# Optimization experiments

Hardware: AMD Instinct MI355X
Metric: run time of the kernel (lower is better)

The kernel has to match this reference:

```python
import jax, jax.numpy as jnp
import numpy as np

EMBED = 1024
HEAD = 64
CTX = 2048


def setup_inputs() -> dict:
    key = jax.random.key(0)
    ks = jax.random.split(key, 7)
    scale = 1.0 / np.sqrt(EMBED)
    return {
        "x": jax.random.normal(ks[0], (8, CTX, EMBED), dtype=jnp.float32),
        "Wq": jax.random.normal(ks[1], (EMBED, HEAD), dtype=jnp.float32) * scale,
        "bq": jax.random.normal(ks[2], (HEAD,), dtype=jnp.float32) * 0.01,
        "Wk": jax.random.normal(ks[3], (EMBED, HEAD), dtype=jnp.float32) * scale,
        "bk": jax.random.normal(ks[4], (HEAD,), dtype=jnp.float32) * 0.01,
        "Wv": jax.random.normal(ks[5], (EMBED, HEAD), dtype=jnp.float32) * scale,
        "bv": jax.random.normal(ks[6], (HEAD,), dtype=jnp.float32) * 0.01,
    }


def reference(x, Wq, bq, Wk, bk, Wv, bv):
    # x: [B, T, E]
    q = x @ Wq + bq  # [B, T, H]
    k = x @ Wk + bk
    v = x @ Wv + bv
    scores = jnp.einsum("bqh,bkh->bqk", q, k) / jnp.sqrt(jnp.float32(HEAD))
    T = x.shape[1]
    causal = jnp.tril(jnp.ones((T, T), dtype=bool))
    scores = jnp.where(causal, scores, -jnp.inf)
    attn = jax.nn.softmax(scores, axis=-1)  # dropout=0.0 -> identity
    out = jnp.einsum("bqk,bkh->bqh", attn, v)
    return out
```

## Files before the change

kernel.cpp:

```cpp
#include <hip/hip_runtime.h>
#include <math.h>
#include <stdint.h>

#define BDIM 8
#define TDIM 2048
#define EDIM 1024
#define HDIM 64
#define NCHUNK 144

typedef short bf16x8 __attribute__((ext_vector_type(8)));
typedef float f32x4 __attribute__((ext_vector_type(4)));

__device__ __forceinline__ unsigned short f2bf(float f) {
    uint32_t u = __builtin_bit_cast(uint32_t, f);
    u += 0x7fffu + ((u >> 16) & 1u);
    return (unsigned short)(u >> 16);
}

__global__ __launch_bounds__(256) void prep_w(
    const float* __restrict__ Wq, const float* __restrict__ Wk,
    const float* __restrict__ Wv,
    unsigned short* __restrict__ WqT, unsigned short* __restrict__ WkT,
    unsigned short* __restrict__ WvT)
{
    int id = blockIdx.x * 256 + threadIdx.x;
    int e = id >> 6, h = id & 63;
    int oi = h * EDIM + e;
    WqT[oi] = f2bf(Wq[id]);
    WkT[oi] = f2bf(Wk[id]);
    WvT[oi] = f2bf(Wv[id]);
}

__global__ __launch_bounds__(256) void proj_kernel(
    const float* __restrict__ x,
    const unsigned short* __restrict__ WqT, const unsigned short* __restrict__ WkT,
    const unsigned short* __restrict__ WvT,
    const float* __restrict__ bq, const float* __restrict__ bk,
    const float* __restrict__ bv,
    unsigned short* __restrict__ Qb, unsigned short* __restrict__ Kb,
    unsigned short* __restrict__ VbT)
{
    __shared__ unsigned short Xs[64][72];
    __shared__ unsigned short Wqs[64][72];
    __shared__ unsigned short Wks[64][72];
    __shared__ unsigned short Wvs[64][72];

    const int t = threadIdx.x;
    const int lane = t & 63, w = t >> 6, quad = lane >> 4, ln = lane & 15;
    const int row0 = blockIdx.x * 64;
    const int sr = t >> 2;
    const int sc = (t & 3) << 4;

    f32x4 accq[4], acck[4], accv[4];
#pragma unroll
    for (int j = 0; j < 4; ++j) {
        accq[j] = (f32x4)(0.f); acck[j] = (f32x4)(0.f); accv[j] = (f32x4)(0.f);
    }

    for (int kt = 0; kt < EDIM / 64; ++kt) {
        __syncthreads();
        const float* xp = &x[(size_t)(row0 + sr) * EDIM + kt * 64 + sc];
        float4 x0 = *(const float4*)(xp);
        float4 x1 = *(const float4*)(xp + 4);
        float4 x2 = *(const float4*)(xp + 8);
        float4 x3 = *(const float4*)(xp + 12);
        bf16x8 xb0, xb1;
        xb0[0]=(short)f2bf(x0.x); xb0[1]=(short)f2bf(x0.y); xb0[2]=(short)f2bf(x0.z); xb0[3]=(short)f2bf(x0.w);
        xb0[4]=(short)f2bf(x1.x); xb0[5]=(short)f2bf(x1.y); xb0[6]=(short)f2bf(x1.z); xb0[7]=(short)f2bf(x1.w);
        xb1[0]=(short)f2bf(x2.x); xb1[1]=(short)f2bf(x2.y); xb1[2]=(short)f2bf(x2.z); xb1[3]=(short)f2bf(x2.w);
        xb1[4]=(short)f2bf(x3.x); xb1[5]=(short)f2bf(x3.y); xb1[6]=(short)f2bf(x3.z); xb1[7]=(short)f2bf(x3.w);
        *(bf16x8*)&Xs[sr][sc]     = xb0;
        *(bf16x8*)&Xs[sr][sc + 8] = xb1;
        size_t wo = (size_t)sr * EDIM + kt * 64 + sc;
        *(bf16x8*)&Wqs[sr][sc]     = *(const bf16x8*)&WqT[wo];
        *(bf16x8*)&Wqs[sr][sc + 8] = *(const bf16x8*)&WqT[wo + 8];
        *(bf16x8*)&Wks[sr][sc]     = *(const bf16x8*)&WkT[wo];
        *(bf16x8*)&Wks[sr][sc + 8] = *(const bf16x8*)&WkT[wo + 8];
        *(bf16x8*)&Wvs[sr][sc]     = *(const bf16x8*)&WvT[wo];
        *(bf16x8*)&Wvs[sr][sc + 8] = *(const bf16x8*)&WvT[wo + 8];
        __syncthreads();

        bf16x8 xa0 = *(const bf16x8*)&Xs[16 * w + ln][8 * quad];
        bf16x8 xa1 = *(const bf16x8*)&Xs[16 * w + ln][32 + 8 * quad];
#pragma unroll
        for (int j = 0; j < 4; ++j) {
            bf16x8 w0, w1;
            w0 = *(const bf16x8*)&Wqs[16 * j + ln][8 * quad];
            w1 = *(const bf16x8*)&Wqs[16 * j + ln][32 + 8 * quad];
            accq[j] = __builtin_amdgcn_mfma_f32_16x16x32_bf16(xa0, w0, accq[j], 0, 0, 0);
            accq[j] = __builtin_amdgcn_mfma_f32_16x16x32_bf16(xa1, w1, accq[j], 0, 0, 0);
            w0 = *(const bf16x8*)&Wks[16 * j + ln][8 * quad];
            w1 = *(const bf16x8*)&Wks[16 * j + ln][32 + 8 * quad];
            acck[j] = __builtin_amdgcn_mfma_f32_16x16x32_bf16(xa0, w0, acck[j], 0, 0, 0);
            acck[j] = __builtin_amdgcn_mfma_f32_16x16x32_bf16(xa1, w1, acck[j], 0, 0, 0);
            w0 = *(const bf16x8*)&Wvs[16 * j + ln][8 * quad];
            w1 = *(const bf16x8*)&Wvs[16 * j + ln][32 + 8 * quad];
            accv[j] = __builtin_amdgcn_mfma_f32_16x16x32_bf16(xa0, w0, accv[j], 0, 0, 0);
            accv[j] = __builtin_amdgcn_mfma_f32_16x16x32_bf16(xa1, w1, accv[j], 0, 0, 0);
        }
    }

#pragma unroll
    for (int j = 0; j < 4; ++j) {
        int col = 16 * j + ln;
        float bqv = bq[col], bkv = bk[col], bvv = bv[col];
#pragma unroll
        for (int r = 0; r < 4; ++r) {
            size_t row = (size_t)(row0 + 16 * w + 4 * quad + r);
            Qb[row * HDIM + col] = f2bf(accq[j][r] + bqv);
            Kb[row * HDIM + col] = f2bf(acck[j][r] + bkv);
            int bb = (int)(row >> 11);
            int tr = (int)(row & 2047);
            VbT[((size_t)bb * HDIM + col) * TDIM + tr] = f2bf(accv[j][r] + bvv);
        }
    }
}

__global__ __launch_bounds__(256) void attn_partial(
    const unsigned short* __restrict__ Qb, const unsigned short* __restrict__ Kb,
    const unsigned short* __restrict__ VbT,
    float* __restrict__ PO, float* __restrict__ Pm, float* __restrict__ Pl)
{
    __shared__ unsigned short Ks[64][72];
    __shared__ unsigned short VsT[64][72];
    __shared__ unsigned short Ps[64][72];

    const int t = threadIdx.x;
    const int lane = t & 63, w = t >> 6, quad = lane >> 4, ln = lane & 15;
    const int f = blockIdx.x;
    const int b = blockIdx.y;

    int g = 0;
    while (f >= 2 * (g + 1) * (g + 2)) ++g;
    const int r_  = f - 2 * g * (g + 1);
    const int iq  = 4 * g + r_ / (g + 1);
    const int ch  = r_ % (g + 1);

    const int q0 = iq * 64;
    const size_t base = (size_t)b * TDIM * HDIM;
    const int sr = t >> 2;
    const int sc = (t & 3) << 4;

    const size_t qrow = base + (size_t)(q0 + 16 * w + ln) * HDIM;
    bf16x8 qa0 = *(const bf16x8*)&Qb[qrow + 8 * quad];
    bf16x8 qa1 = *(const bf16x8*)&Qb[qrow + 32 + 8 * quad];

    f32x4 od[4];
#pragma unroll
    for (int j = 0; j < 4; ++j) od[j] = (f32x4)(0.f);
    float mrow[4], lrow[4];
#pragma unroll
    for (int r = 0; r < 4; ++r) { mrow[r] = -INFINITY; lrow[r] = 0.f; }

    const float scale = 0.125f;
    int j1 = 4 * ch + 3; if (j1 > iq) j1 = iq;

    for (int jt = 4 * ch; jt <= j1; ++jt) {
        __syncthreads();
        {
            size_t ko = base + (size_t)(jt * 64 + sr) * HDIM + sc;
            *(bf16x8*)&Ks[sr][sc]     = *(const bf16x8*)&Kb[ko];
            *(bf16x8*)&Ks[sr][sc + 8] = *(const bf16x8*)&Kb[ko + 8];
            const unsigned short* vrow =
                &VbT[((size_t)b * HDIM + sr) * TDIM + jt * 64 + sc];
            *(bf16x8*)&VsT[sr][sc]     = *(const bf16x8*)vrow;
            *(bf16x8*)&VsT[sr][sc + 8] = *(const bf16x8*)(vrow + 8);
        }
        __syncthreads();

        f32x4 s[4];
#pragma unroll
        for (int j = 0; j < 4; ++j) {
            bf16x8 kb0 = *(const bf16x8*)&Ks[16 * j + ln][8 * quad];
            bf16x8 kb1 = *(const bf16x8*)&Ks[16 * j + ln][32 + 8 * quad];
            s[j] = (f32x4)(0.f);
            s[j] = __builtin_amdgcn_mfma_f32_16x16x32_bf16(qa0, kb0, s[j], 0, 0, 0);
            s[j] = __builtin_amdgcn_mfma_f32_16x16x32_bf16(qa1, kb1, s[j], 0, 0, 0);
        }

        if (jt == iq) {
#pragma unroll
            for (int j = 0; j < 4; ++j) {
                int kg = jt * 64 + 16 * j + ln;
#pragma unroll
                for (int r = 0; r < 4; ++r) {
                    int qg = q0 + 16 * w + 4 * quad + r;
                    s[j][r] = (kg <= qg) ? s[j][r] * scale : -INFINITY;
                }
            }
        } else {
#pragma unroll
            for (int j = 0; j < 4; ++j)
#pragma unroll
                for (int r = 0; r < 4; ++r) s[j][r] *= scale;
        }

        float mx[4];
#pragma unroll
        for (int r = 0; r < 4; ++r)
            mx[r] = fmaxf(fmaxf(s[0][r], s[1][r]), fmaxf(s[2][r], s[3][r]));
#pragma unroll
        for (int d = 1; d < 16; d <<= 1)
#pragma unroll
            for (int r = 0; r < 4; ++r)
                mx[r] = fmaxf(mx[r], __shfl_xor(mx[r], d));

        float al[4], rs[4];
#pragma unroll
        for (int r = 0; r < 4; ++r) {
            float mn = fmaxf(mrow[r], mx[r]);
            al[r] = __expf(mrow[r] - mn);
            mrow[r] = mn;
            float p0 = __expf(s[0][r] - mn);
            float p1 = __expf(s[1][r] - mn);
            float p2 = __expf(s[2][r] - mn);
            float p3 = __expf(s[3][r] - mn);
            s[0][r] = p0; s[1][r] = p1; s[2][r] = p2; s[3][r] = p3;
            rs[r] = (p0 + p1) + (p2 + p3);
        }
#pragma unroll
        for (int d = 1; d < 16; d <<= 1)
#pragma unroll
            for (int r = 0; r < 4; ++r)
                rs[r] += __shfl_xor(rs[r], d);
#pragma unroll
        for (int r = 0; r < 4; ++r) lrow[r] = lrow[r] * al[r] + rs[r];

#pragma unroll
        for (int j = 0; j < 4; ++j)
#pragma unroll
            for (int r = 0; r < 4; ++r) {
                od[j][r] *= al[r];
                Ps[16 * w + 4 * quad + r][16 * j + ln] = f2bf(s[j][r]);
            }

        bf16x8 pa0 = *(const bf16x8*)&Ps[16 * w + ln][8 * quad];
        bf16x8 pa1 = *(const bf16x8*)&Ps[16 * w + ln][32 + 8 * quad];
#pragma unroll
        for (int j = 0; j < 4; ++j) {
            bf16x8 vb0 = *(const bf16x8*)&VsT[16 * j + ln][8 * quad];
            bf16x8 vb1 = *(const bf16x8*)&VsT[16 * j + ln][32 + 8 * quad];
            od[j] = __builtin_amdgcn_mfma_f32_16x16x32_bf16(pa0, vb0, od[j], 0, 0, 0);
            od[j] = __builtin_amdgcn_mfma_f32_16x16x32_bf16(pa1, vb1, od[j], 0, 0, 0);
        }
    }

    const size_t p = (size_t)b * NCHUNK + f;
#pragma unroll
    for (int j = 0; j < 4; ++j)
#pragma unroll
        for (int r = 0; r < 4; ++r)
            PO[p * 4096 + (size_t)(16 * w + 4 * quad + r) * 64 + 16 * j + ln] = od[j][r];
    if (ln == 0) {
#pragma unroll
        for (int r = 0; r < 4; ++r) {
            Pm[p * 64 + 16 * w + 4 * quad + r] = mrow[r];
            Pl[p * 64 + 16 * w + 4 * quad + r] = lrow[r];
        }
    }
}

__global__ __launch_bounds__(256) void attn_combine(
    const float* __restrict__ PO, const float* __restrict__ Pm,
    const float* __restrict__ Pl, float* __restrict__ out)
{
    const int iq = blockIdx.x, b = blockIdx.y;
    const int g = iq >> 2;
    const int nch = g + 1;
    const int fbase = 2 * g * (g + 1) + (iq - 4 * g) * (g + 1);
    const int t = threadIdx.x;
    const int row = t >> 2;
    const int c0 = (t & 3) << 4;
    const size_t pbase = (size_t)b * NCHUNK + fbase;

    float M = -INFINITY;
    for (int c = 0; c < nch; ++c)
        M = fmaxf(M, Pm[(pbase + c) * 64 + row]);

    float4 a0 = {0,0,0,0}, a1 = {0,0,0,0}, a2 = {0,0,0,0}, a3 = {0,0,0,0};
    float L = 0.f;
    for (int c = 0; c < nch; ++c) {
        size_t p = pbase + c;
        float sc = __expf(Pm[p * 64 + row] - M);
        L += sc * Pl[p * 64 + row];
        const float* po = &PO[p * 4096 + (size_t)row * 64 + c0];
        float4 v0 = *(const float4*)(po);
        float4 v1 = *(const float4*)(po + 4);
        float4 v2 = *(const float4*)(po + 8);
        float4 v3 = *(const float4*)(po + 12);
        a0.x += sc*v0.x; a0.y += sc*v0.y; a0.z += sc*v0.z; a0.w += sc*v0.w;
        a1.x += sc*v1.x; a1.y += sc*v1.y; a1.z += sc*v1.z; a1.w += sc*v1.w;
        a2.x += sc*v2.x; a2.y += sc*v2.y; a2.z += sc*v2.z; a2.w += sc*v2.w;
        a3.x += sc*v3.x; a3.y += sc*v3.y; a3.z += sc*v3.z; a3.w += sc*v3.w;
    }
    float li = 1.f / L;
    a0.x*=li; a0.y*=li; a0.z*=li; a0.w*=li;
    a1.x*=li; a1.y*=li; a1.z*=li; a1.w*=li;
    a2.x*=li; a2.y*=li; a2.z*=li; a2.w*=li;
    a3.x*=li; a3.y*=li; a3.z*=li; a3.w*=li;
    float* op = &out[((size_t)b * TDIM + (size_t)iq * 64 + row) * HDIM + c0];
    *(float4*)(op)      = a0;
    *(float4*)(op + 4)  = a1;
    *(float4*)(op + 8)  = a2;
    *(float4*)(op + 12) = a3;
}

extern "C" void kernel_launch(void* const* d_in, const int* in_sizes, int n_in,
                              void* d_out, int out_size, void* d_ws, size_t ws_size,
                              hipStream_t stream) {
    const float* x  = (const float*)d_in[0];
    const float* Wq = (const float*)d_in[1];
    const float* bq = (const float*)d_in[2];
    const float* Wk = (const float*)d_in[3];
    const float* bk = (const float*)d_in[4];
    const float* Wv = (const float*)d_in[5];
    const float* bv = (const float*)d_in[6];
    float* out = (float*)d_out;

    const size_t n = (size_t)BDIM * TDIM * HDIM;
    unsigned short* Qb  = (unsigned short*)d_ws;
    unsigned short* Kb  = Qb + n;
    unsigned short* VbT = Kb + n;
    unsigned short* WqT = VbT + n;
    unsigned short* WkT = WqT + (size_t)EDIM * HDIM;
    unsigned short* WvT = WkT + (size_t)EDIM * HDIM;
    float* PO = (float*)(WvT + (size_t)EDIM * HDIM);
    float* Pm = PO + (size_t)BDIM * NCHUNK * 4096;
    float* Pl = Pm + (size_t)BDIM * NCHUNK * 64;

    prep_w<<<dim3(EDIM * HDIM / 256), 256, 0, stream>>>(Wq, Wk, Wv, WqT, WkT, WvT);
    proj_kernel<<<dim3(BDIM * TDIM / 64), 256, 0, stream>>>(
        x, WqT, WkT, WvT, bq, bk, bv, Qb, Kb, VbT);
    attn_partial<<<dim3(NCHUNK, BDIM), 256, 0, stream>>>(Qb, Kb, VbT, PO, Pm, Pl);
    attn_combine<<<dim3(TDIM / 64, BDIM), 256, 0, stream>>>(PO, Pm, Pl, out);
}
```

Before: 156.6 us.

## Bypass LDS for weights and K/V, double-buffer X tiles in projection

The projection kernel now reads bf16 weight fragments straight from global memory (relying on cache hits) instead of staging them through LDS. The X tile is double-buffered in LDS, with the next tile prefetched into registers while the current one is used, so each iteration needs one barrier instead of two. The attention kernel also loads K and V^T fragments directly from global memory per wave, which removes both block barriers per key tile. The cost is redundant global/L1 traffic, since every wave re-reads the same weight, K and V data, and more load latency is exposed to the MFMA loop.

```diff
diff --git a/kernel.cpp b/kernel.cpp
--- a/kernel.cpp
+++ b/kernel.cpp
@@ -40,10 +40,7 @@
     unsigned short* __restrict__ Qb, unsigned short* __restrict__ Kb,
     unsigned short* __restrict__ VbT)
 {
-    __shared__ unsigned short Xs[64][72];
-    __shared__ unsigned short Wqs[64][72];
-    __shared__ unsigned short Wks[64][72];
-    __shared__ unsigned short Wvs[64][72];
+    __shared__ unsigned short Xs[2][64][72];
 
     const int t = threadIdx.x;
     const int lane = t & 63, w = t >> 6, quad = lane >> 4, ln = lane & 15;
@@ -57,9 +54,8 @@
         accq[j] = (f32x4)(0.f); acck[j] = (f32x4)(0.f); accv[j] = (f32x4)(0.f);
     }
 
-    for (int kt = 0; kt < EDIM / 64; ++kt) {
-        __syncthreads();
-        const float* xp = &x[(size_t)(row0 + sr) * EDIM + kt * 64 + sc];
+    {
+        const float* xp = &x[(size_t)(row0 + sr) * EDIM + sc];
         float4 x0 = *(const float4*)(xp);
         float4 x1 = *(const float4*)(xp + 4);
         float4 x2 = *(const float4*)(xp + 8);
@@ -69,34 +65,54 @@
         xb0[4]=(short)f2bf(x1.x); xb0[5]=(short)f2bf(x1.y); xb0[6]=(short)f2bf(x1.z); xb0[7]=(short)f2bf(x1.w);
         xb1[0]=(short)f2bf(x2.x); xb1[1]=(short)f2bf(x2.y); xb1[2]=(short)f2bf(x2.z); xb1[3]=(short)f2bf(x2.w);
         xb1[4]=(short)f2bf(x3.x); xb1[5]=(short)f2bf(x3.y); xb1[6]=(short)f2bf(x3.z); xb1[7]=(short)f2bf(x3.w);
-        *(bf16x8*)&Xs[sr][sc]     = xb0;
-        *(bf16x8*)&Xs[sr][sc + 8] = xb1;
-        size_t wo = (size_t)sr * EDIM + kt * 64 + sc;
-        *(bf16x8*)&Wqs[sr][sc]     = *(const bf16x8*)&WqT[wo];
-        *(bf16x8*)&Wqs[sr][sc + 8] = *(const bf16x8*)&WqT[wo + 8];
-        *(bf16x8*)&Wks[sr][sc]     = *(const bf16x8*)&WkT[wo];
-        *(bf16x8*)&Wks[sr][sc + 8] = *(const bf16x8*)&WkT[wo + 8];
-        *(bf16x8*)&Wvs[sr][sc]     = *(const bf16x8*)&WvT[wo];
-        *(bf16x8*)&Wvs[sr][sc + 8] = *(const bf16x8*)&WvT[wo + 8];
+        *(bf16x8*)&Xs[0][sr][sc]     = xb0;
+        *(bf16x8*)&Xs[0][sr][sc + 8] = xb1;
+    }
+
+    for (int kt = 0; kt < EDIM / 64; ++kt) {
+        const int cur = kt & 1, nxt = cur ^ 1;
+
+        float4 x0, x1, x2, x3;
+        if (kt < 15) {
+            const float* xp = &x[(size_t)(row0 + sr) * EDIM + (kt + 1) * 64 + sc];
+            x0 = *(const float4*)(xp);
+            x1 = *(const float4*)(xp + 4);
+            x2 = *(const float4*)(xp + 8);
+            x3 = *(const float4*)(xp + 12);
+        }
+
         __syncthreads();
 
-        bf16x8 xa0 = *(const bf16x8*)&Xs[16 * w + ln][8 * quad];
-        bf16x8 xa1 = *(const bf16x8*)&Xs[16 * w + ln][32 + 8 * quad];
+        bf16x8 xa0 = *(const bf16x8*)&Xs[cur][16 * w + ln][8 * quad];
+        bf16x8 xa1 = *(const bf16x8*)&Xs[cur][16 * w + ln][32 + 8 * quad];
+
+        const size_t wkb = (size_t)kt * 64 + 8 * quad;
 #pragma unroll
         for (int j = 0; j < 4; ++j) {
+            const size_t wrow = (size_t)(16 * j + ln) * EDIM + wkb;
             bf16x8 w0, w1;
-            w0 = *(const bf16x8*)&Wqs[16 * j + ln][8 * quad];
-            w1 = *(const bf16x8*)&Wqs[16 * j + ln][32 + 8 * quad];
+            w0 = *(const bf16x8*)&WqT[wrow];
+            w1 = *(const bf16x8*)&WqT[wrow + 32];
             accq[j] = __builtin_amdgcn_mfma_f32_16x16x32_bf16(xa0, w0, accq[j], 0, 0, 0);
             accq[j] = __builtin_amdgcn_mfma_f32_16x16x32_bf16(xa1, w1, accq[j], 0, 0, 0);
-            w0 = *(const bf16x8*)&Wks[16 * j + ln][8 * quad];
-            w1 = *(const bf16x8*)&Wks[16 * j + ln][32 + 8 * quad];
+            w0 = *(const bf16x8*)&WkT[wrow];
+            w1 = *(const bf16x8*)&WkT[wrow + 32];
             acck[j] = __builtin_amdgcn_mfma_f32_16x16x32_bf16(xa0, w0, acck[j], 0, 0, 0);
             acck[j] = __builtin_amdgcn_mfma_f32_16x16x32_bf16(xa1, w1, acck[j], 0, 0, 0);
-            w0 = *(const bf16x8*)&Wvs[16 * j + ln][8 * quad];
-            w1 = *(const bf16x8*)&Wvs[16 * j + ln][32 + 8 * quad];
+            w0 = *(const bf16x8*)&WvT[wrow];
+            w1 = *(const bf16x8*)&WvT[wrow + 32];
             accv[j] = __builtin_amdgcn_mfma_f32_16x16x32_bf16(xa0, w0, accv[j], 0, 0, 0);
             accv[j] = __builtin_amdgcn_mfma_f32_16x16x32_bf16(xa1, w1, accv[j], 0, 0, 0);
+        }
+
+        if (kt < 15) {
+            bf16x8 xb0, xb1;
+            xb0[0]=(short)f2bf(x0.x); xb0[1]=(short)f2bf(x0.y); xb0[2]=(short)f2bf(x0.z); xb0[3]=(short)f2bf(x0.w);
+            xb0[4]=(short)f2bf(x1.x); xb0[5]=(short)f2bf(x1.y); xb0[6]=(short)f2bf(x1.z); xb0[7]=(short)f2bf(x1.w);
+            xb1[0]=(short)f2bf(x2.x); xb1[1]=(short)f2bf(x2.y); xb1[2]=(short)f2bf(x2.z); xb1[3]=(short)f2bf(x2.w);
+            xb1[4]=(short)f2bf(x3.x); xb1[5]=(short)f2bf(x3.y); xb1[6]=(short)f2bf(x3.z); xb1[7]=(short)f2bf(x3.w);
+            *(bf16x8*)&Xs[nxt][sr][sc]     = xb0;
+            *(bf16x8*)&Xs[nxt][sr][sc + 8] = xb1;
         }
     }
 
@@ -121,8 +137,6 @@
     const unsigned short* __restrict__ VbT,
     float* __restrict__ PO, float* __restrict__ Pm, float* __restrict__ Pl)
 {
-    __shared__ unsigned short Ks[64][72];
-    __shared__ unsigned short VsT[64][72];
     __shared__ unsigned short Ps[64][72];
 
     const int t = threadIdx.x;
@@ -138,8 +152,6 @@
 
     const int q0 = iq * 64;
     const size_t base = (size_t)b * TDIM * HDIM;
-    const int sr = t >> 2;
-    const int sc = (t & 3) << 4;
 
     const size_t qrow = base + (size_t)(q0 + 16 * w + ln) * HDIM;
     bf16x8 qa0 = *(const bf16x8*)&Qb[qrow + 8 * quad];
@@ -156,23 +168,12 @@
     int j1 = 4 * ch + 3; if (j1 > iq) j1 = iq;
 
     for (int jt = 4 * ch; jt <= j1; ++jt) {
-        __syncthreads();
-        {
-            size_t ko = base + (size_t)(jt * 64 + sr) * HDIM + sc;
-            *(bf16x8*)&Ks[sr][sc]     = *(const bf16x8*)&Kb[ko];
-            *(bf16x8*)&Ks[sr][sc + 8] = *(const bf16x8*)&Kb[ko + 8];
-            const unsigned short* vrow =
-                &VbT[((size_t)b * HDIM + sr) * TDIM + jt * 64 + sc];
-            *(bf16x8*)&VsT[sr][sc]     = *(const bf16x8*)vrow;
-            *(bf16x8*)&VsT[sr][sc + 8] = *(const bf16x8*)(vrow + 8);
-        }
-        __syncthreads();
-
         f32x4 s[4];
 #pragma unroll
         for (int j = 0; j < 4; ++j) {
-            bf16x8 kb0 = *(const bf16x8*)&Ks[16 * j + ln][8 * quad];
-            bf16x8 kb1 = *(const bf16x8*)&Ks[16 * j + ln][32 + 8 * quad];
+            const size_t krow = base + (size_t)(jt * 64 + 16 * j + ln) * HDIM;
+            bf16x8 kb0 = *(const bf16x8*)&Kb[krow + 8 * quad];
+            bf16x8 kb1 = *(const bf16x8*)&Kb[krow + 32 + 8 * quad];
             s[j] = (f32x4)(0.f);
             s[j] = __builtin_amdgcn_mfma_f32_16x16x32_bf16(qa0, kb0, s[j], 0, 0, 0);
             s[j] = __builtin_amdgcn_mfma_f32_16x16x32_bf16(qa1, kb1, s[j], 0, 0, 0);
@@ -238,8 +239,9 @@
         bf16x8 pa1 = *(const bf16x8*)&Ps[16 * w + ln][32 + 8 * quad];
 #pragma unroll
         for (int j = 0; j < 4; ++j) {
-            bf16x8 vb0 = *(const bf16x8*)&VsT[16 * j + ln][8 * quad];
-            bf16x8 vb1 = *(const bf16x8*)&VsT[16 * j + ln][32 + 8 * quad];
+            const size_t vrow = ((size_t)b * HDIM + 16 * j + ln) * TDIM + jt * 64;
+            bf16x8 vb0 = *(const bf16x8*)&VbT[vrow + 8 * quad];
+            bf16x8 vb1 = *(const bf16x8*)&VbT[vrow + 32 + 8 * quad];
             od[j] = __builtin_amdgcn_mfma_f32_16x16x32_bf16(pa0, vb0, od[j], 0, 0, 0);
             od[j] = __builtin_amdgcn_mfma_f32_16x16x32_bf16(pa1, vb1, od[j], 0, 0, 0);
         }
```

After: 203.4 us. 1.3x slower.
